# Optimization experiments

Hardware: AMD Instinct MI355X
Metric: run time of the kernel (lower is better)

The kernel has to match this reference:

```python
import jax, jax.numpy as jnp
import numpy as np

E = 1024
H = 16
D = E // H  # head_dim = 64
FF = 4 * E
EPS = 1e-5


def layernorm(x, g, b):
    mu = jnp.mean(x, axis=-1, keepdims=True)
    var = jnp.var(x, axis=-1, keepdims=True)
    return (x - mu) * jax.lax.rsqrt(var + EPS) * g + b


def setup_inputs() -> dict:
    key = jax.random.key(0)
    ks = jax.random.split(key, 12)
    s = 1.0 / np.sqrt(E)
    sf = 1.0 / np.sqrt(FF)
    return {
        "x": jax.random.normal(ks[0], (2, 2048, E), dtype=jnp.float32),
        "wq": jax.random.uniform(ks[1], (E, E), jnp.float32, -s, s),
        "wk": jax.random.uniform(ks[2], (E, E), jnp.float32, -s, s),
        "wv": jax.random.uniform(ks[3], (E, E), jnp.float32, -s, s),
        "wo": jax.random.uniform(ks[4], (E, E), jnp.float32, -s, s),
        "bo": jax.random.uniform(ks[5], (E,), jnp.float32, -s, s),
        "g1": jnp.ones((E,), jnp.float32),
        "b1": jnp.zeros((E,), jnp.float32),
        "w1": jax.random.uniform(ks[6], (FF, E), jnp.float32, -s, s),
        "bf1": jax.random.uniform(ks[7], (FF,), jnp.float32, -s, s),
        "w2": jax.random.uniform(ks[8], (E, FF), jnp.float32, -sf, sf),
        "bf2": jax.random.uniform(ks[9], (E,), jnp.float32, -sf, sf),
        "g2": jnp.ones((E,), jnp.float32),
        "b2": jnp.zeros((E,), jnp.float32),
    }


def reference(x, wq, wk, wv, wo, bo, g1, b1, w1, bf1, w2, bf2, g2, b2):
    B, L, _ = x.shape
    # projections (torch Linear: x @ W.T)
    q = (x @ wq.T).reshape(B, L, H, D).transpose(0, 2, 1, 3)  # (B,H,L,D)
    k = (x @ wk.T).reshape(B, L, H, D).transpose(0, 2, 1, 3)
    v = (x @ wv.T).reshape(B, L, H, D).transpose(0, 2, 1, 3)
    scores = jnp.einsum('bhqd,bhkd->bhqk', q, k) / np.sqrt(D)
    attn = jax.nn.softmax(scores, axis=-1)
    ctx = jnp.einsum('bhqk,bhkd->bhqd', attn, v)
    ctx = ctx.transpose(0, 2, 1, 3).reshape(B, L, E)
    attn_out = ctx @ wo.T + bo
    h = layernorm(x + attn_out, g1, b1)
    ff = jax.nn.gelu(h @ w1.T + bf1, approximate=False) @ w2.T + bf2
    return layernorm(h + ff, g2, b2)
```

## Files before the change

kernel.cpp:

```cpp
#include <hip/hip_runtime.h>
#include <hip/hip_bf16.h>
#include <stdint.h>

typedef __bf16 bf16x8 __attribute__((ext_vector_type(8)));
typedef float  f32x4  __attribute__((ext_vector_type(4)));
typedef unsigned short u16;
typedef u16 u16x8 __attribute__((ext_vector_type(8)));

__device__ __forceinline__ u16 f2b(float f) {
  uint32_t u = __builtin_bit_cast(uint32_t, f);
  u += 0x7fffu + ((u >> 16) & 1u);
  return (u16)(u >> 16);
}

__device__ __forceinline__ f32x4 mfma16(bf16x8 a, bf16x8 b, f32x4 c) {
  return __builtin_amdgcn_mfma_f32_16x16x32_bf16(a, b, c, 0, 0, 0);
}

__device__ __forceinline__ void gload_lds16(const void* g, void* l) {
  __builtin_amdgcn_global_load_lds(
      (const __attribute__((address_space(1))) void*)g,
      (__attribute__((address_space(3))) void*)l, 16, 0, 0);
}

__global__ void f2b_conv(const float* __restrict__ in, u16* __restrict__ out, int n8) {
  const int i = blockIdx.x * blockDim.x + threadIdx.x;
  if (i >= n8) return;
  const float4* p = (const float4*)in + (size_t)i * 2;
  float4 a = p[0], b = p[1];
  u16x8 r;
  r[0] = f2b(a.x); r[1] = f2b(a.y); r[2] = f2b(a.z); r[3] = f2b(a.w);
  r[4] = f2b(b.x); r[5] = f2b(b.y); r[6] = f2b(b.z); r[7] = f2b(b.w);
  *((u16x8*)out + i) = r;
}

template<int MODE>
__global__ __launch_bounds__(256, 3) void gemm_bt(
    const u16* __restrict__ A, const u16* __restrict__ W,
    const float* __restrict__ bias,
    void* __restrict__ o0, void* __restrict__ o1, void* __restrict__ o2,
    int Nsz, int Kstride, int Klen, int ntiles)
{
  __shared__ u16 As[2][128 * 32];
  __shared__ u16 Bs[2][128 * 32];
  const int nbn = Nsz >> 7;
  int bid = blockIdx.x;
  bid = (bid & 7) * ((int)gridDim.x >> 3) + (bid >> 3);
  const int tile = (MODE == 1) ? (bid % ntiles) : bid;
  const int sid  = (MODE == 1) ? (bid / ntiles) : 0;
  const int koff = sid * Klen;
  const int bm = tile / nbn;
  const int bn = tile % nbn;
  const int tid = threadIdx.x;
  const int w = tid >> 6, l = tid & 63;
  const int lh = l >> 4, ll = l & 15;
  const int wr = w >> 1, wc = w & 1;

  f32x4 acc[4][4] = {};

  const u16* Ag = A + (size_t)(bm * 128) * Kstride + koff;
  const u16* Wg = W + (size_t)(bn * 128) * Kstride + koff;

  const int flat0 = (w * 2) * 64 + l;
  const int flat1 = (w * 2 + 1) * 64 + l;

  {
    gload_lds16(Ag + (size_t)(flat0 >> 2) * Kstride + (flat0 & 3) * 8, As[0] + flat0 * 8);
    gload_lds16(Wg + (size_t)(flat0 >> 2) * Kstride + (flat0 & 3) * 8, Bs[0] + flat0 * 8);
    gload_lds16(Ag + (size_t)(flat1 >> 2) * Kstride + (flat1 & 3) * 8, As[0] + flat1 * 8);
    gload_lds16(Wg + (size_t)(flat1 >> 2) * Kstride + (flat1 & 3) * 8, Bs[0] + flat1 * 8);
  }
  __syncthreads();

  const int NS = Klen >> 5;
  int buf = 0;
  for (int s = 0; s < NS; ++s) {
    if (s + 1 < NS) {
      const int k0 = (s + 1) * 32;
      gload_lds16(Ag + (size_t)(flat0 >> 2) * Kstride + k0 + (flat0 & 3) * 8, As[buf ^ 1] + flat0 * 8);
      gload_lds16(Wg + (size_t)(flat0 >> 2) * Kstride + k0 + (flat0 & 3) * 8, Bs[buf ^ 1] + flat0 * 8);
      gload_lds16(Ag + (size_t)(flat1 >> 2) * Kstride + k0 + (flat1 & 3) * 8, As[buf ^ 1] + flat1 * 8);
      gload_lds16(Wg + (size_t)(flat1 >> 2) * Kstride + k0 + (flat1 & 3) * 8, Bs[buf ^ 1] + flat1 * 8);
    }
    bf16x8 af[4], bfr[4];
#pragma unroll
    for (int mi = 0; mi < 4; ++mi)
      af[mi] = *(const bf16x8*)(As[buf] + (wr * 64 + mi * 16 + ll) * 32 + lh * 8);
#pragma unroll
    for (int ni = 0; ni < 4; ++ni)
      bfr[ni] = *(const bf16x8*)(Bs[buf] + (wc * 64 + ni * 16 + ll) * 32 + lh * 8);
    __builtin_amdgcn_s_setprio(1);
#pragma unroll
    for (int mi = 0; mi < 4; ++mi)
#pragma unroll
      for (int ni = 0; ni < 4; ++ni)
        acc[mi][ni] = mfma16(af[mi], bfr[ni], acc[mi][ni]);
    __builtin_amdgcn_s_setprio(0);
    __syncthreads();
    buf ^= 1;
  }

#pragma unroll
  for (int mi = 0; mi < 4; ++mi) {
#pragma unroll
    for (int ni = 0; ni < 4; ++ni) {
      const int col = bn * 128 + wc * 64 + ni * 16 + ll;
#pragma unroll
      for (int i = 0; i < 4; ++i) {
        const int row = bm * 128 + wr * 64 + mi * 16 + lh * 4 + i;
        float v = acc[mi][ni][i];
        if (MODE == 1) {
          float* dst = sid ? (float*)o1 : (float*)o0;
          dst[(size_t)row * Nsz + col] = v;
        } else if (MODE == 2) {
          float xx = v + bias[col];
          float gl = 0.5f * xx * (1.0f + erff(xx * 0.70710678118654752f));
          ((u16*)o0)[(size_t)row * Nsz + col] = f2b(gl);
        } else {
          const int which = col >> 10;
          const int e = col & 1023;
          const int hh = e >> 6, dd = e & 63;
          const int bb = row >> 11, nl = row & 2047;
          if (which == 0) {
            ((u16*)o0)[((size_t)(bb * 16 + hh) * 2048 + nl) * 64 + dd] = f2b(v * 0.18033688f);
          } else if (which == 1) {
            ((u16*)o1)[((size_t)(bb * 16 + hh) * 2048 + nl) * 64 + dd] = f2b(v);
          } else {
            ((u16*)o2)[((size_t)(bb * 16 + hh) * 64 + dd) * 2048 + nl] = f2b(v);
          }
        }
      }
    }
  }
}

__global__ __launch_bounds__(256, 4) void attn_fwd(
    const u16* __restrict__ Q, const u16* __restrict__ K,
    const u16* __restrict__ Vt, u16* __restrict__ ctx)
{
  __shared__ u16 Ks[2][64 * 64];
  __shared__ u16 Vs[2][64 * 64];
  __shared__ u16 Ps[4][16 * 64];

  const int bh = blockIdx.x & 31;
  const int qt = blockIdx.x >> 5;
  const int tid = threadIdx.x;
  const int w = tid >> 6, l = tid & 63;
  const int lh = l >> 4, ll = l & 15;
  const int q0 = qt * 64 + w * 16;

  bf16x8 qf[2];
  {
    const u16* Qg = Q + ((size_t)bh * 2048 + q0 + ll) * 64;
#pragma unroll
    for (int kk = 0; kk < 2; ++kk)
      qf[kk] = *(const bf16x8*)(Qg + kk * 32 + lh * 8);
  }

  bf16x8 ones;
  {
    const u16 o = 0x3F80;
#pragma unroll
    for (int i = 0; i < 8; ++i) ones[i] = __builtin_bit_cast(__bf16, o);
  }

  f32x4 cacc[4] = {};
  f32x4 lacc = {};
  float m_l = -1e30f;
  u16* ps = Ps[w];

  const int f0 = tid, f1 = 256 + tid;
  const int r0 = f0 >> 3, s0 = f0 & 7, g0 = (s0 ^ (r0 & 7)) * 8;
  const int r1 = f1 >> 3, s1 = f1 & 7, g1 = (s1 ^ (r1 & 7)) * 8;

  {
    gload_lds16(K + ((size_t)bh * 2048 + r0) * 64 + g0, Ks[0] + f0 * 8);
    gload_lds16(Vt + ((size_t)bh * 64 + r0) * 2048 + g0, Vs[0] + f0 * 8);
    gload_lds16(K + ((size_t)bh * 2048 + r1) * 64 + g1, Ks[0] + f1 * 8);
    gload_lds16(Vt + ((size_t)bh * 64 + r1) * 2048 + g1, Vs[0] + f1 * 8);
  }
  __syncthreads();

  for (int kt = 0; kt < 32; ++kt) {
    const int b = kt & 1;
    if (kt < 31) {
      const int kn = (kt + 1) * 64;
      gload_lds16(K + ((size_t)bh * 2048 + kn + r0) * 64 + g0, Ks[b ^ 1] + f0 * 8);
      gload_lds16(Vt + ((size_t)bh * 64 + r0) * 2048 + kn + g0, Vs[b ^ 1] + f0 * 8);
      gload_lds16(K + ((size_t)bh * 2048 + kn + r1) * 64 + g1, Ks[b ^ 1] + f1 * 8);
      gload_lds16(Vt + ((size_t)bh * 64 + r1) * 2048 + kn + g1, Vs[b ^ 1] + f1 * 8);
    }

    f32x4 st[4];
    __builtin_amdgcn_s_setprio(1);
#pragma unroll
    for (int jb = 0; jb < 4; ++jb) {
      f32x4 a = {};
#pragma unroll
      for (int kk = 0; kk < 2; ++kk) {
        const int r = jb * 16 + ll;
        bf16x8 kf = *(const bf16x8*)(Ks[b] + r * 64 + (((kk * 4 + lh) ^ (r & 7)) * 8));
        a = mfma16(kf, qf[kk], a);
      }
      st[jb] = a;
    }
    __builtin_amdgcn_s_setprio(0);

    float mx = fmaxf(fmaxf(fmaxf(st[0][0], st[0][1]), fmaxf(st[0][2], st[0][3])),
                     fmaxf(fmaxf(st[1][0], st[1][1]), fmaxf(st[1][2], st[1][3])));
    mx = fmaxf(mx, fmaxf(fmaxf(fmaxf(st[2][0], st[2][1]), fmaxf(st[2][2], st[2][3])),
                         fmaxf(fmaxf(st[3][0], st[3][1]), fmaxf(st[3][2], st[3][3]))));
    mx = fmaxf(mx, __shfl_xor(mx, 16));
    mx = fmaxf(mx, __shfl_xor(mx, 32));

    if (!__all(mx - m_l <= 8.0f)) {
      const float mn = fmaxf(m_l, mx);
      const float al = __builtin_amdgcn_exp2f(m_l - mn);
      m_l = mn;
      float alq[4];
#pragma unroll
      for (int i = 0; i < 4; ++i) alq[i] = __shfl(al, lh * 4 + i);
#pragma unroll
      for (int db = 0; db < 4; ++db)
#pragma unroll
        for (int i = 0; i < 4; ++i) cacc[db][i] *= alq[i];
#pragma unroll
      for (int i = 0; i < 4; ++i) lacc[i] *= alq[i];
    }

#pragma unroll
    for (int jb = 0; jb < 4; ++jb) {
      const float p0 = __builtin_amdgcn_exp2f(st[jb][0] - m_l);
      const float p1 = __builtin_amdgcn_exp2f(st[jb][1] - m_l);
      const float p2 = __builtin_amdgcn_exp2f(st[jb][2] - m_l);
      const float p3 = __builtin_amdgcn_exp2f(st[jb][3] - m_l);
      uint2 pk;
      asm("v_cvt_pk_bf16_f32 %0, %1, %2" : "=v"(pk.x) : "v"(p0), "v"(p1));
      asm("v_cvt_pk_bf16_f32 %0, %1, %2" : "=v"(pk.y) : "v"(p2), "v"(p3));
      *(uint2*)(ps + ll * 64 + (((jb * 2 + (lh >> 1)) ^ (ll & 7)) * 8) + (lh & 1) * 4) = pk;
    }

    asm volatile("s_waitcnt lgkmcnt(0)" ::: "memory");
    __builtin_amdgcn_sched_barrier(0);

    __builtin_amdgcn_s_setprio(1);
#pragma unroll
    for (int kk = 0; kk < 2; ++kk) {
      bf16x8 pf = *(const bf16x8*)(ps + ll * 64 + (((kk * 4 + lh) ^ (ll & 7)) * 8));
      lacc = mfma16(pf, ones, lacc);
#pragma unroll
      for (int db = 0; db < 4; ++db) {
        const int vr = db * 16 + ll;
        bf16x8 vf = *(const bf16x8*)(Vs[b] + vr * 64 + (((kk * 4 + lh) ^ (vr & 7)) * 8));
        cacc[db] = mfma16(pf, vf, cacc[db]);
      }
    }
    __builtin_amdgcn_s_setprio(0);
    __syncthreads();
  }

  const int bb = bh >> 4, hh = bh & 15;
#pragma unroll
  for (int db = 0; db < 4; ++db)
#pragma unroll
    for (int i = 0; i < 4; ++i) {
      const float v = cacc[db][i] / lacc[i];
      const size_t orow = (size_t)bb * 2048 + q0 + lh * 4 + i;
      const size_t ocol = (size_t)hh * 64 + db * 16 + ll;
      ctx[orow * 1024 + ocol] = f2b(v);
    }
}

__global__ __launch_bounds__(256) void ln_fused(
    const float* __restrict__ a, const float* __restrict__ b0,
    const float* __restrict__ b1, const float* __restrict__ bias,
    const float* __restrict__ g, const float* __restrict__ be,
    float* __restrict__ ho, u16* __restrict__ hb)
{
  const int row = blockIdx.x;
  const int t = threadIdx.x;
  const size_t base = (size_t)row * 1024 + t * 4;
  float4 xa = *(const float4*)(a + base);
  float4 xb = *(const float4*)(b0 + base);
  float v0 = xa.x + xb.x, v1 = xa.y + xb.y, v2 = xa.z + xb.z, v3 = xa.w + xb.w;
  if (b1) {
    float4 xc = *(const float4*)(b1 + base);
    v0 += xc.x; v1 += xc.y; v2 += xc.z; v3 += xc.w;
  }
  if (bias) {
    float4 xd = *(const float4*)(bias + t * 4);
    v0 += xd.x; v1 += xd.y; v2 += xd.z; v3 += xd.w;
  }
  float s = v0 + v1 + v2 + v3;
  float ss = v0 * v0 + v1 * v1 + v2 * v2 + v3 * v3;
#pragma unroll
  for (int d = 1; d < 64; d <<= 1) {
    s += __shfl_xor(s, d);
    ss += __shfl_xor(ss, d);
  }
  __shared__ float red[8];
  const int w = t >> 6, lid = t & 63;
  if (lid == 0) { red[w] = s; red[4 + w] = ss; }
  __syncthreads();
  s = red[0] + red[1] + red[2] + red[3];
  ss = red[4] + red[5] + red[6] + red[7];
  const float mean = s * (1.0f / 1024.0f);
  const float var = ss * (1.0f / 1024.0f) - mean * mean;
  const float rstd = rsqrtf(var + 1e-5f);
  const float vv[4] = {v0, v1, v2, v3};
#pragma unroll
  for (int i = 0; i < 4; ++i) {
    const int col = t * 4 + i;
    const float hv = (vv[i] - mean) * rstd * g[col] + be[col];
    if (ho) ho[base + i] = hv;
    if (hb) hb[base + i] = f2b(hv);
  }
}

extern "C" void kernel_launch(void* const* d_in, const int* in_sizes, int n_in,
                              void* d_out, int out_size, void* d_ws, size_t ws_size,
                              hipStream_t stream) {
  const float* x   = (const float*)d_in[0];
  const float* wq  = (const float*)d_in[1];
  const float* wk  = (const float*)d_in[2];
  const float* wv  = (const float*)d_in[3];
  const float* wo  = (const float*)d_in[4];
  const float* bo  = (const float*)d_in[5];
  const float* g1  = (const float*)d_in[6];
  const float* b1  = (const float*)d_in[7];
  const float* w1  = (const float*)d_in[8];
  const float* bf1 = (const float*)d_in[9];
  const float* w2  = (const float*)d_in[10];
  const float* bf2 = (const float*)d_in[11];
  const float* g2  = (const float*)d_in[12];
  const float* b2  = (const float*)d_in[13];

  char* ws = (char*)d_ws;
  const size_t MB = 1u << 20;
  u16* xb    = (u16*)(ws + 0);
  u16* wqkv  = (u16*)(ws + 8 * MB);
  u16* wob   = (u16*)(ws + 14 * MB);
  u16* w1b   = (u16*)(ws + 16 * MB);
  u16* w2b   = (u16*)(ws + 24 * MB);
  u16* qb    = (u16*)(ws + 32 * MB);
  u16* kb    = (u16*)(ws + 40 * MB);
  u16* vtb   = (u16*)(ws + 48 * MB);
  u16* ctxb  = (u16*)(ws + 56 * MB);
  float* p0buf = (float*)(ws + 64 * MB);
  float* hbuf  = (float*)(ws + 80 * MB);
  u16* hbb   = (u16*)(ws + 96 * MB);
  float* wo_p1 = (float*)(ws + 32 * MB);
  float* f2_p1 = (float*)(ws + 0);
  u16* ff1   = (u16*)(ws + 32 * MB);

  f2b_conv<<<2048, 256, 0, stream>>>(x, xb, 524288);
  f2b_conv<<<512, 256, 0, stream>>>(wq, wqkv, 131072);
  f2b_conv<<<512, 256, 0, stream>>>(wk, wqkv + 1048576, 131072);
  f2b_conv<<<512, 256, 0, stream>>>(wv, wqkv + 2097152, 131072);
  f2b_conv<<<512, 256, 0, stream>>>(wo, wob, 131072);
  f2b_conv<<<2048, 256, 0, stream>>>(w1, w1b, 524288);
  f2b_conv<<<2048, 256, 0, stream>>>(w2, w2b, 524288);

  gemm_bt<0><<<768, 256, 0, stream>>>(xb, wqkv, nullptr, qb, kb, vtb, 3072, 1024, 1024, 768);
  attn_fwd<<<1024, 256, 0, stream>>>(qb, kb, vtb, ctxb);
  gemm_bt<1><<<512, 256, 0, stream>>>(ctxb, wob, nullptr, p0buf, wo_p1, nullptr, 1024, 1024, 512, 256);
  ln_fused<<<4096, 256, 0, stream>>>(x, p0buf, wo_p1, bo, g1, b1, hbuf, hbb);
  gemm_bt<2><<<1024, 256, 0, stream>>>(hbb, w1b, bf1, ff1, nullptr, nullptr, 4096, 1024, 1024, 1024);
  gemm_bt<1><<<512, 256, 0, stream>>>(ff1, w2b, nullptr, p0buf, f2_p1, nullptr, 1024, 4096, 2048, 256);
  ln_fused<<<4096, 256, 0, stream>>>(hbuf, p0buf, f2_p1, bf2, g2, b2, (float*)d_out, nullptr);
}
```

Baseline: 277.9 us.

## Switch GEMMs to 256x256 tiles with 4-stage LDS pipeline and swizzle

Replaces the 128x128 double-buffered GEMM with a 512-thread 256x256 tile kernel. It uses a 4-deep global_load_lds ring with explicit vmcnt waits and an XOR-swizzled LDS layout to cut bank conflicts and raise data reuse per load. The seven conversion launches are merged into one kernel. The FF2 GEMM now uses split-K 4, with its partials summed in the final layernorm. The larger tiles use far more LDS and give fewer blocks (128–256), so some GEMMs may leave CUs idle. One partial buffer reuses the output buffer.

```diff
diff --git a/kernel.cpp b/kernel.cpp
--- a/kernel.cpp
+++ b/kernel.cpp
@@ -23,27 +23,44 @@
       (__attribute__((address_space(3))) void*)l, 16, 0, 0);
 }
 
-__global__ void f2b_conv(const float* __restrict__ in, u16* __restrict__ out, int n8) {
+#define BARRIER() asm volatile("s_barrier" ::: "memory")
+
+__global__ void f2b_all(const float* __restrict__ x,  const float* __restrict__ wq,
+                        const float* __restrict__ wk, const float* __restrict__ wv,
+                        const float* __restrict__ wo, const float* __restrict__ w1,
+                        const float* __restrict__ w2,
+                        u16* __restrict__ xb, u16* __restrict__ wqkvb,
+                        u16* __restrict__ wob, u16* __restrict__ w1b,
+                        u16* __restrict__ w2b) {
   const int i = blockIdx.x * blockDim.x + threadIdx.x;
-  if (i >= n8) return;
-  const float4* p = (const float4*)in + (size_t)i * 2;
+  const float* src; u16* dst; int off;
+  if (i < 524288)        { src = x;  dst = xb;              off = i; }
+  else if (i < 655360)   { src = wq; dst = wqkvb;           off = i - 524288; }
+  else if (i < 786432)   { src = wk; dst = wqkvb + 1048576; off = i - 655360; }
+  else if (i < 917504)   { src = wv; dst = wqkvb + 2097152; off = i - 786432; }
+  else if (i < 1048576)  { src = wo; dst = wob;             off = i - 917504; }
+  else if (i < 1572864)  { src = w1; dst = w1b;             off = i - 1048576; }
+  else                   { src = w2; dst = w2b;             off = i - 1572864; }
+  const float4* p = (const float4*)src + (size_t)off * 2;
   float4 a = p[0], b = p[1];
   u16x8 r;
   r[0] = f2b(a.x); r[1] = f2b(a.y); r[2] = f2b(a.z); r[3] = f2b(a.w);
   r[4] = f2b(b.x); r[5] = f2b(b.y); r[6] = f2b(b.z); r[7] = f2b(b.w);
-  *((u16x8*)out + i) = r;
+  *((u16x8*)dst + off) = r;
 }
 
 template<int MODE>
-__global__ __launch_bounds__(256, 3) void gemm_bt(
+__global__ __launch_bounds__(512, 2) void gemm256(
     const u16* __restrict__ A, const u16* __restrict__ W,
     const float* __restrict__ bias,
-    void* __restrict__ o0, void* __restrict__ o1, void* __restrict__ o2,
+    void* __restrict__ o0, void* __restrict__ o1,
+    void* __restrict__ o2, void* __restrict__ o3,
     int Nsz, int Kstride, int Klen, int ntiles)
 {
-  __shared__ u16 As[2][128 * 32];
-  __shared__ u16 Bs[2][128 * 32];
-  const int nbn = Nsz >> 7;
+  __shared__ u16 As[4][256 * 32];
+  __shared__ u16 Bs[4][256 * 32];
+
+  const int nbn = Nsz >> 8;
   int bid = blockIdx.x;
   bid = (bid & 7) * ((int)gridDim.x >> 3) + (bid >> 3);
   const int tile = (MODE == 1) ? (bid % ntiles) : bid;
@@ -54,63 +71,78 @@
   const int tid = threadIdx.x;
   const int w = tid >> 6, l = tid & 63;
   const int lh = l >> 4, ll = l & 15;
-  const int wr = w >> 1, wc = w & 1;
-
-  f32x4 acc[4][4] = {};
-
-  const u16* Ag = A + (size_t)(bm * 128) * Kstride + koff;
-  const u16* Wg = W + (size_t)(bn * 128) * Kstride + koff;
-
-  const int flat0 = (w * 2) * 64 + l;
-  const int flat1 = (w * 2 + 1) * 64 + l;
-
-  {
-    gload_lds16(Ag + (size_t)(flat0 >> 2) * Kstride + (flat0 & 3) * 8, As[0] + flat0 * 8);
-    gload_lds16(Wg + (size_t)(flat0 >> 2) * Kstride + (flat0 & 3) * 8, Bs[0] + flat0 * 8);
-    gload_lds16(Ag + (size_t)(flat1 >> 2) * Kstride + (flat1 & 3) * 8, As[0] + flat1 * 8);
-    gload_lds16(Wg + (size_t)(flat1 >> 2) * Kstride + (flat1 & 3) * 8, Bs[0] + flat1 * 8);
-  }
-  __syncthreads();
-
-  const int NS = Klen >> 5;
-  int buf = 0;
-  for (int s = 0; s < NS; ++s) {
-    if (s + 1 < NS) {
-      const int k0 = (s + 1) * 32;
-      gload_lds16(Ag + (size_t)(flat0 >> 2) * Kstride + k0 + (flat0 & 3) * 8, As[buf ^ 1] + flat0 * 8);
-      gload_lds16(Wg + (size_t)(flat0 >> 2) * Kstride + k0 + (flat0 & 3) * 8, Bs[buf ^ 1] + flat0 * 8);
-      gload_lds16(Ag + (size_t)(flat1 >> 2) * Kstride + k0 + (flat1 & 3) * 8, As[buf ^ 1] + flat1 * 8);
-      gload_lds16(Wg + (size_t)(flat1 >> 2) * Kstride + k0 + (flat1 & 3) * 8, Bs[buf ^ 1] + flat1 * 8);
-    }
-    bf16x8 af[4], bfr[4];
-#pragma unroll
-    for (int mi = 0; mi < 4; ++mi)
-      af[mi] = *(const bf16x8*)(As[buf] + (wr * 64 + mi * 16 + ll) * 32 + lh * 8);
-#pragma unroll
-    for (int ni = 0; ni < 4; ++ni)
-      bfr[ni] = *(const bf16x8*)(Bs[buf] + (wc * 64 + ni * 16 + ll) * 32 + lh * 8);
+  const int wm = w >> 2, wn = w & 3;
+
+  f32x4 acc[8][4] = {};
+
+  const u16* Ag = A + (size_t)(bm * 256) * Kstride + koff;
+  const u16* Wg = W + (size_t)(bn * 256) * Kstride + koff;
+
+  const int r0 = tid >> 2;
+  const int sg = (tid & 3) ^ ((r0 >> 1) & 3);
+  const int NT = Klen >> 5;
+
+  auto issue = [&](int t) {
+    const int b = t & 3;
+    const size_t kk = (size_t)t * 32 + sg * 8;
+    gload_lds16(Ag + (size_t)r0 * Kstride + kk,         As[b] + tid * 8);
+    gload_lds16(Ag + (size_t)(r0 + 128) * Kstride + kk, As[b] + (512 + tid) * 8);
+    gload_lds16(Wg + (size_t)r0 * Kstride + kk,         Bs[b] + tid * 8);
+    gload_lds16(Wg + (size_t)(r0 + 128) * Kstride + kk, Bs[b] + (512 + tid) * 8);
+  };
+
+  auto compute_tile = [&](int t) {
+    const u16* As_b = As[t & 3];
+    const u16* Bs_b = Bs[t & 3];
+    bf16x8 bfv[4], af[8];
+#pragma unroll
+    for (int ni = 0; ni < 4; ++ni) {
+      const int r = wn * 64 + ni * 16 + ll;
+      bfv[ni] = *(const bf16x8*)(Bs_b + r * 32 + ((lh ^ ((r >> 1) & 3)) * 8));
+    }
+#pragma unroll
+    for (int mi = 0; mi < 8; ++mi) {
+      const int r = wm * 128 + mi * 16 + ll;
+      af[mi] = *(const bf16x8*)(As_b + r * 32 + ((lh ^ ((r >> 1) & 3)) * 8));
+    }
     __builtin_amdgcn_s_setprio(1);
 #pragma unroll
-    for (int mi = 0; mi < 4; ++mi)
+    for (int mi = 0; mi < 8; ++mi)
 #pragma unroll
       for (int ni = 0; ni < 4; ++ni)
-        acc[mi][ni] = mfma16(af[mi], bfr[ni], acc[mi][ni]);
+        acc[mi][ni] = mfma16(af[mi], bfv[ni], acc[mi][ni]);
     __builtin_amdgcn_s_setprio(0);
-    __syncthreads();
-    buf ^= 1;
-  }
-
-#pragma unroll
-  for (int mi = 0; mi < 4; ++mi) {
+  };
+
+  issue(0); issue(1); issue(2);
+
+  int t = 0;
+  for (; t < NT - 3; ++t) {
+    issue(t + 3);
+    asm volatile("s_waitcnt vmcnt(12)" ::: "memory");
+    BARRIER();
+    compute_tile(t);
+    BARRIER();
+  }
+  asm volatile("s_waitcnt vmcnt(8)" ::: "memory");
+  BARRIER(); compute_tile(t); BARRIER(); ++t;
+  asm volatile("s_waitcnt vmcnt(4)" ::: "memory");
+  BARRIER(); compute_tile(t); BARRIER(); ++t;
+  asm volatile("s_waitcnt vmcnt(0)" ::: "memory");
+  BARRIER(); compute_tile(t);
+
+#pragma unroll
+  for (int mi = 0; mi < 8; ++mi) {
 #pragma unroll
     for (int ni = 0; ni < 4; ++ni) {
-      const int col = bn * 128 + wc * 64 + ni * 16 + ll;
+      const int col = bn * 256 + wn * 64 + ni * 16 + ll;
 #pragma unroll
       for (int i = 0; i < 4; ++i) {
-        const int row = bm * 128 + wr * 64 + mi * 16 + lh * 4 + i;
+        const int row = bm * 256 + wm * 128 + mi * 16 + lh * 4 + i;
         float v = acc[mi][ni][i];
         if (MODE == 1) {
-          float* dst = sid ? (float*)o1 : (float*)o0;
+          float* dst = (sid == 0) ? (float*)o0 : (sid == 1) ? (float*)o1
+                     : (sid == 2) ? (float*)o2 : (float*)o3;
           dst[(size_t)row * Nsz + col] = v;
         } else if (MODE == 2) {
           float xx = v + bias[col];
@@ -272,9 +304,10 @@
 }
 
 __global__ __launch_bounds__(256) void ln_fused(
-    const float* __restrict__ a, const float* __restrict__ b0,
-    const float* __restrict__ b1, const float* __restrict__ bias,
-    const float* __restrict__ g, const float* __restrict__ be,
+    const float* __restrict__ a,  const float* __restrict__ b0,
+    const float* __restrict__ b1, const float* __restrict__ b2,
+    const float* __restrict__ b3, const float* __restrict__ bias,
+    const float* __restrict__ g,  const float* __restrict__ be,
     float* __restrict__ ho, u16* __restrict__ hb)
 {
   const int row = blockIdx.x;
@@ -285,6 +318,14 @@
   float v0 = xa.x + xb.x, v1 = xa.y + xb.y, v2 = xa.z + xb.z, v3 = xa.w + xb.w;
   if (b1) {
     float4 xc = *(const float4*)(b1 + base);
+    v0 += xc.x; v1 += xc.y; v2 += xc.z; v3 += xc.w;
+  }
+  if (b2) {
+    float4 xc = *(const float4*)(b2 + base);
+    v0 += xc.x; v1 += xc.y; v2 += xc.z; v3 += xc.w;
+  }
+  if (b3) {
+    float4 xc = *(const float4*)(b3 + base);
     v0 += xc.x; v1 += xc.y; v2 += xc.z; v3 += xc.w;
   }
   if (bias) {
@@ -346,26 +387,27 @@
   u16* kb    = (u16*)(ws + 40 * MB);
   u16* vtb   = (u16*)(ws + 48 * MB);
   u16* ctxb  = (u16*)(ws + 56 * MB);
-  float* p0buf = (float*)(ws + 64 * MB);
-  float* hbuf  = (float*)(ws + 80 * MB);
+  float* pA   = (float*)(ws + 64 * MB);
+  float* hbuf = (float*)(ws + 80 * MB);
   u16* hbb   = (u16*)(ws + 96 * MB);
   float* wo_p1 = (float*)(ws + 32 * MB);
+  u16* ff1   = (u16*)(ws + 32 * MB);
   float* f2_p1 = (float*)(ws + 0);
-  u16* ff1   = (u16*)(ws + 32 * MB);
-
-  f2b_conv<<<2048, 256, 0, stream>>>(x, xb, 524288);
-  f2b_conv<<<512, 256, 0, stream>>>(wq, wqkv, 131072);
-  f2b_conv<<<512, 256, 0, stream>>>(wk, wqkv + 1048576, 131072);
-  f2b_conv<<<512, 256, 0, stream>>>(wv, wqkv + 2097152, 131072);
-  f2b_conv<<<512, 256, 0, stream>>>(wo, wob, 131072);
-  f2b_conv<<<2048, 256, 0, stream>>>(w1, w1b, 524288);
-  f2b_conv<<<2048, 256, 0, stream>>>(w2, w2b, 524288);
-
-  gemm_bt<0><<<768, 256, 0, stream>>>(xb, wqkv, nullptr, qb, kb, vtb, 3072, 1024, 1024, 768);
+  float* f2_p2 = (float*)(ws + 48 * MB);
+  float* f2_p3 = (float*)d_out;
+
+  f2b_all<<<8192, 256, 0, stream>>>(x, wq, wk, wv, wo, w1, w2, xb, wqkv, wob, w1b, w2b);
+
+  gemm256<0><<<192, 512, 0, stream>>>(xb, wqkv, nullptr, qb, kb, vtb, nullptr,
+                                      3072, 1024, 1024, 0);
   attn_fwd<<<1024, 256, 0, stream>>>(qb, kb, vtb, ctxb);
-  gemm_bt<1><<<512, 256, 0, stream>>>(ctxb, wob, nullptr, p0buf, wo_p1, nullptr, 1024, 1024, 512, 256);
-  ln_fused<<<4096, 256, 0, stream>>>(x, p0buf, wo_p1, bo, g1, b1, hbuf, hbb);
-  gemm_bt<2><<<1024, 256, 0, stream>>>(hbb, w1b, bf1, ff1, nullptr, nullptr, 4096, 1024, 1024, 1024);
-  gemm_bt<1><<<512, 256, 0, stream>>>(ff1, w2b, nullptr, p0buf, f2_p1, nullptr, 1024, 4096, 2048, 256);
-  ln_fused<<<4096, 256, 0, stream>>>(hbuf, p0buf, f2_p1, bf2, g2, b2, (float*)d_out, nullptr);
-}
+  gemm256<1><<<128, 512, 0, stream>>>(ctxb, wob, nullptr, pA, wo_p1, nullptr, nullptr,
+                                      1024, 1024, 512, 64);
+  ln_fused<<<4096, 256, 0, stream>>>(x, pA, wo_p1, nullptr, nullptr, bo, g1, b1, hbuf, hbb);
+  gemm256<2><<<256, 512, 0, stream>>>(hbb, w1b, bf1, ff1, nullptr, nullptr, nullptr,
+                                      4096, 1024, 1024, 0);
+  gemm256<1><<<256, 512, 0, stream>>>(ff1, w2b, nullptr, pA, f2_p1, f2_p2, f2_p3,
+                                      1024, 4096, 1024, 64);
+  ln_fused<<<4096, 256, 0, stream>>>(hbuf, pA, f2_p1, f2_p2, f2_p3, bf2, g2, b2,
+                                     (float*)d_out, nullptr);
+}
```

After: 314.5 us. 13.2% more time.
